# Optimization experiments

Hardware: AMD Instinct MI355X
Metric: run time of the kernel (lower is better)

The kernel has to match this reference:

```python
import jax, jax.numpy as jnp
import numpy as np

B, D, H, W, N = 64, 512, 32, 32, 20
E = 512  # emb_size
TEMP = 10.0


def setup_inputs() -> dict:
    key = jax.random.key(0)
    ks = jax.random.split(key, 16)
    inp = {
        "fvisu": jax.random.normal(ks[0], (B, D, H, W), jnp.float32),
        "fword": jax.random.normal(ks[1], (B, N, D), jnp.float32),
        "context_score": jax.random.uniform(ks[2], (B, N), jnp.float32),
        "fcoord": jax.random.normal(ks[3], (B, 8, H, W), jnp.float32),
        "gest": jax.random.normal(ks[4], (B, 8), jnp.float32),
        "word_mask": jax.random.randint(ks[5], (B, N), 0, 2, jnp.int32),
        # parameters (kaiming-uniform-ish scale)
        "attn_map_w": jax.random.normal(ks[6], (E // 2, D), jnp.float32) * (1.0 / np.sqrt(D)),
        "attn_map_b": jnp.zeros((E // 2,), jnp.float32),
        "attn_score_w": jax.random.normal(ks[7], (1, E // 2), jnp.float32) * (1.0 / np.sqrt(E // 2)),
        "attn_score_b": jnp.zeros((1,), jnp.float32),
        "gamma_w": jax.random.normal(ks[8], (2 * E, D), jnp.float32) * (1.0 / np.sqrt(D)),
        "gamma_b": jnp.zeros((2 * E,), jnp.float32),
        "conv1_w": jax.random.normal(ks[9], (E, D + 8), jnp.float32) * (1.0 / np.sqrt(D + 8)),
        "conv1_b": jnp.zeros((E,), jnp.float32),
    }
    return inp


def mask_softmax(attn_score, word_mask, temp=TEMP):
    # score: (B, N)
    score = jax.nn.softmax(attn_score * temp, axis=1)
    m = word_mask.astype(jnp.int32)
    m = m.at[:, 0].set(0)                      # zero CLS position
    idx = jnp.sum(m, axis=1)                   # index of SEP (post-CLS-zeroing), matches torch loop
    m = m.at[jnp.arange(m.shape[0]), idx].set(0)
    ms = score * m.astype(score.dtype)
    return ms / (jnp.sum(ms, axis=1, keepdims=True) + 1e-8)


def reference(fvisu, fword, context_score, fcoord, gest, word_mask,
              attn_map_w, attn_map_b, attn_score_w, attn_score_b,
              gamma_w, gamma_b, conv1_w, conv1_b):
    # fword: (B, N, D) -> module permutes to (B, D, N)
    fw = jnp.transpose(fword, (0, 2, 1))                      # (B, D, N)
    tile_visu = jnp.mean(fvisu.reshape(B, D, -1), axis=2, keepdims=True)  # (B, D, 1)
    context_tile = tile_visu * fw * context_score[:, None, :]  # (B, D, N)

    # 1x1 Conv1d -> GEMM
    attn_feat = jnp.tanh(jnp.einsum('od,bdn->bon', attn_map_w, context_tile)
                         + attn_map_b[None, :, None])          # (B, E/2, N)
    attn_score = (jnp.einsum('oc,bcn->bon', attn_score_w, attn_feat)[:, 0, :]
                  + attn_score_b[0])                           # (B, N)

    mask_score = mask_softmax(attn_score, word_mask)            # (B, N)
    attn_lang = jnp.einsum('bn,bnd->bd', mask_score, fword)     # (B, D)

    # FiLM parameter decode
    film = attn_lang @ gamma_w.T + gamma_b                      # (B, 2E)
    gammas = jnp.tanh(film[:, :E])[:, :, None, None]
    betas = jnp.tanh(film[:, E:])[:, :, None, None]

    # 1x1 Conv2d on concat(fvisu, fcoord) + InstanceNorm2d (no affine, eps=1e-5)
    x = jnp.concatenate([fvisu, fcoord], axis=1)                # (B, D+8, H, W)
    conv = jnp.einsum('oc,bchw->bohw', conv1_w, x) + conv1_b[None, :, None, None]
    mu = jnp.mean(conv, axis=(2, 3), keepdims=True)
    var = jnp.var(conv, axis=(2, 3), keepdims=True)
    norm = (conv - mu) * jax.lax.rsqrt(var + 1e-5)

    fmodu = jax.nn.relu(gammas * norm + betas)
    fmodu = fvisu + fmodu
    return fmodu, attn_lang, attn_score
```

## Files before the change

### kernel.cpp

```cpp
#include <hip/hip_runtime.h>
#include <math.h>

#define BB 64
#define DD 512
#define HW 1024
#define NN 20
#define EE 512
#define CIN 520
#define KCN 17
#define TEMP_F 10.0f

#define OUT_ALANG (BB*DD*HW)
#define OUT_ASCORE (OUT_ALANG + BB*DD)

typedef __bf16 bf16x8 __attribute__((ext_vector_type(8)));
typedef float f32x4 __attribute__((ext_vector_type(4)));

__device__ __forceinline__ unsigned int pack2bf(float a, float b) {
    unsigned int ua = __builtin_bit_cast(unsigned int, a);
    unsigned int ub = __builtin_bit_cast(unsigned int, b);
    ua += 0x7fffu + ((ua >> 16) & 1u);
    ub += 0x7fffu + ((ub >> 16) & 1u);
    return (ua >> 16) | (ub & 0xffff0000u);
}

__device__ __forceinline__ unsigned short bfr(float x) {
    unsigned int u = __builtin_bit_cast(unsigned int, x);
    u += 0x7fffu + ((u >> 16) & 1u);
    return (unsigned short)(u >> 16);
}

__device__ __forceinline__ float bf2f(unsigned short u) {
    unsigned int x = ((unsigned int)u) << 16;
    return __builtin_bit_cast(float, x);
}

__global__ __launch_bounds__(256) void k_tilevisu(const float* __restrict__ fvisu,
                                                  float* __restrict__ tv) {
    int row = blockIdx.x;
    const float4* p = (const float4*)(fvisu + (size_t)row * HW);
    int tid = threadIdx.x;
    float4 v = p[tid];
    float s = v.x + v.y + v.z + v.w;
    #pragma unroll
    for (int off = 32; off; off >>= 1) s += __shfl_down(s, off, 64);
    __shared__ float part[4];
    if ((tid & 63) == 0) part[tid >> 6] = s;
    __syncthreads();
    if (tid == 0) tv[row] = (part[0] + part[1] + part[2] + part[3]) * (1.0f / HW);
}

__global__ __launch_bounds__(512) void k_convert_x(
    const float* __restrict__ fvisu, const float* __restrict__ fcoord,
    unsigned short* __restrict__ Xf, float* __restrict__ tv) {
    int L = blockIdx.x;
    int kc = L % KCN;
    int b  = L / KCN;
    int t = threadIdx.x;
    int co = t >> 7;
    int tl = t & 127;
    int cbase = kc * 32 + co * 8;
    float sums[8];
    #pragma unroll
    for (int j = 0; j < 8; ++j) sums[j] = 0.f;

    #pragma unroll
    for (int i = 0; i < 2; ++i) {
        int p0 = (tl + 128 * i) * 4;
        float4 f4[8];
        #pragma unroll
        for (int j = 0; j < 8; ++j) {
            int c = cbase + j;
            if (c < DD) {
                f4[j] = *(const float4*)&fvisu[((size_t)b * DD + c) * HW + p0];
            } else if (c < CIN) {
                f4[j] = *(const float4*)&fcoord[((size_t)b * 8 + (c - DD)) * HW + p0];
            } else {
                f4[j] = make_float4(0.f, 0.f, 0.f, 0.f);
            }
        }
        #pragma unroll
        for (int j = 0; j < 8; ++j)
            if (cbase + j < DD) sums[j] += f4[j].x + f4[j].y + f4[j].z + f4[j].w;

        size_t base = (((size_t)b * 64 + (p0 >> 4)) * KCN + kc) * 512
                    + (size_t)(co * 16 + (p0 & 15)) * 8;
        #pragma unroll
        for (int i2 = 0; i2 < 4; ++i2) {
            uint4 v;
            v.x = pack2bf(((const float*)&f4[0])[i2], ((const float*)&f4[1])[i2]);
            v.y = pack2bf(((const float*)&f4[2])[i2], ((const float*)&f4[3])[i2]);
            v.z = pack2bf(((const float*)&f4[4])[i2], ((const float*)&f4[5])[i2]);
            v.w = pack2bf(((const float*)&f4[6])[i2], ((const float*)&f4[7])[i2]);
            *(uint4*)&Xf[base + (size_t)i2 * 8] = v;
        }
    }

    #pragma unroll
    for (int j = 0; j < 8; ++j) {
        float s = sums[j];
        #pragma unroll
        for (int off = 32; off; off >>= 1) s += __shfl_down(s, off, 64);
        sums[j] = s;
    }
    __shared__ float red[8][8];
    int w = t >> 6;
    if ((t & 63) == 0) {
        #pragma unroll
        for (int j = 0; j < 8; ++j) red[w][j] = sums[j];
    }
    __syncthreads();
    if (t < 32) {
        int j = t & 7, c2 = t >> 3;
        int c = kc * 32 + c2 * 8 + j;
        if (c < DD) tv[(size_t)b * DD + c] = (red[c2 * 2][j] + red[c2 * 2 + 1][j]) * (1.0f / HW);
    }
}

__global__ __launch_bounds__(256) void k_convert_w(
    const float* __restrict__ cw, unsigned short* __restrict__ Wf) {
    int t = threadIdx.x;
    int frag = blockIdx.x * 4 + (t >> 6);
    int l = t & 63;
    int M = frag / KCN, kc = frag % KCN;
    int o = M * 16 + (l & 15);
    int k0 = kc * 32 + (l >> 4) * 8;
    float f[8];
    #pragma unroll
    for (int j = 0; j < 8; ++j) {
        int k = k0 + j;
        f[j] = (k < CIN) ? cw[(size_t)o * CIN + k] : 0.f;
    }
    uint4 v;
    v.x = pack2bf(f[0], f[1]);
    v.y = pack2bf(f[2], f[3]);
    v.z = pack2bf(f[4], f[5]);
    v.w = pack2bf(f[6], f[7]);
    *(uint4*)&Wf[(size_t)frag * 512 + (size_t)l * 8] = v;
}

__global__ __launch_bounds__(256) void k_convert_w2(
    const float* __restrict__ amw, unsigned short* __restrict__ Whi,
    unsigned short* __restrict__ Wlo) {
    int t = threadIdx.x;
    int fid = blockIdx.x * 4 + (t >> 6);
    int l = t & 63;
    int ot = fid >> 4, ks = fid & 15;
    int o = ot * 16 + (l & 15);
    int k0 = ks * 32 + ((l >> 4) & 3) * 8;
    float hi[8], lo[8];
    #pragma unroll
    for (int j = 0; j < 8; ++j) {
        float x = amw[(size_t)o * DD + k0 + j];
        unsigned short h = bfr(x);
        hi[j] = bf2f(h);
        lo[j] = x - hi[j];
    }
    uint4 vh, vl;
    vh.x = pack2bf(hi[0], hi[1]); vh.y = pack2bf(hi[2], hi[3]);
    vh.z = pack2bf(hi[4], hi[5]); vh.w = pack2bf(hi[6], hi[7]);
    vl.x = pack2bf(lo[0], lo[1]); vl.y = pack2bf(lo[2], lo[3]);
    vl.z = pack2bf(lo[4], lo[5]); vl.w = pack2bf(lo[6], lo[7]);
    *(uint4*)&Whi[(size_t)fid * 512 + (size_t)l * 8] = vh;
    *(uint4*)&Wlo[(size_t)fid * 512 + (size_t)l * 8] = vl;
}

__global__ __launch_bounds__(256) void k_convert_gwt(
    const float* __restrict__ gw, float* __restrict__ gwT) {
    __shared__ float tile[64][65];
    int bt = blockIdx.x;
    int rt = bt & 15, kt = bt >> 4;
    int t = threadIdx.x;
    int rl = t >> 4;
    int kl = (t & 15) * 4;
    #pragma unroll
    for (int i = 0; i < 4; ++i) {
        int rr = rl + i * 16;
        float4 v = *(const float4*)&gw[(size_t)(rt * 64 + rr) * DD + kt * 64 + kl];
        tile[rr][kl + 0] = v.x; tile[rr][kl + 1] = v.y;
        tile[rr][kl + 2] = v.z; tile[rr][kl + 3] = v.w;
    }
    __syncthreads();
    #pragma unroll
    for (int i = 0; i < 4; ++i) {
        int kk = rl + i * 16;
        float4 v;
        v.x = tile[kl + 0][kk]; v.y = tile[kl + 1][kk];
        v.z = tile[kl + 2][kk]; v.w = tile[kl + 3][kk];
        *(float4*)&gwT[(size_t)(kt * 64 + kk) * 1024 + rt * 64 + kl] = v;
    }
}

__global__ __launch_bounds__(256) void k_attnscore(
    const float* __restrict__ fword, const float* __restrict__ cs,
    const float* __restrict__ tv, const unsigned short* __restrict__ Whi,
    const unsigned short* __restrict__ Wlo, const float* __restrict__ amb,
    const float* __restrict__ asw, const float* __restrict__ asb,
    const int* __restrict__ wmask, float* __restrict__ out_ascore,
    float* __restrict__ out_alang) {
    int b = blockIdx.x;
    __shared__ unsigned short uhi[2][16][64][8];
    __shared__ unsigned short ulo[2][16][64][8];
    __shared__ float scoreP[4][32];
    __shared__ float asc_sh[NN];
    __shared__ float msh[NN];
    int t = threadIdx.x;

    {
        int n = t & 31, kq = t >> 5;
        float csv = (n < NN) ? cs[b * NN + n] : 0.f;
        const float* fwp = fword + ((size_t)b * NN + (n < NN ? n : 0)) * DD;
        const float* tvp = tv + (size_t)b * DD;
        int mt = n >> 4;
        #pragma unroll
        for (int oc = 0; oc < 8; ++oc) {
            int k = kq * 64 + oc * 8;
            float x[8];
            if (n < NN) {
                float4 f0 = *(const float4*)&fwp[k];
                float4 f1 = *(const float4*)&fwp[k + 4];
                float4 t0 = *(const float4*)&tvp[k];
                float4 t1 = *(const float4*)&tvp[k + 4];
                x[0] = f0.x * t0.x * csv; x[1] = f0.y * t0.y * csv;
                x[2] = f0.z * t0.z * csv; x[3] = f0.w * t0.w * csv;
                x[4] = f1.x * t1.x * csv; x[5] = f1.y * t1.y * csv;
                x[6] = f1.z * t1.z * csv; x[7] = f1.w * t1.w * csv;
            } else {
                #pragma unroll
                for (int j = 0; j < 8; ++j) x[j] = 0.f;
            }
            float h[8], lw[8];
            #pragma unroll
            for (int j = 0; j < 8; ++j) {
                h[j] = bf2f(bfr(x[j]));
                lw[j] = x[j] - h[j];
            }
            int ks = k >> 5;
            int l = (n & 15) + ((k >> 3) & 3) * 16;
            uint4 vh, vl;
            vh.x = pack2bf(h[0], h[1]); vh.y = pack2bf(h[2], h[3]);
            vh.z = pack2bf(h[4], h[5]); vh.w = pack2bf(h[6], h[7]);
            vl.x = pack2bf(lw[0], lw[1]); vl.y = pack2bf(lw[2], lw[3]);
            vl.z = pack2bf(lw[4], lw[5]); vl.w = pack2bf(lw[6], lw[7]);
            *(uint4*)&uhi[mt][ks][l][0] = vh;
            *(uint4*)&ulo[mt][ks][l][0] = vl;
        }
    }
    __syncthreads();

    int w = t >> 6, l = t & 63;
    f32x4 acc[2][4];
    #pragma unroll
    for (int mt = 0; mt < 2; ++mt)
        #pragma unroll
        for (int nt = 0; nt < 4; ++nt) acc[mt][nt] = (f32x4){0.f, 0.f, 0.f, 0.f};

    #pragma unroll 4
    for (int ks = 0; ks < 16; ++ks) {
        bf16x8 ah0 = *(const bf16x8*)&uhi[0][ks][l][0];
        bf16x8 ah1 = *(const bf16x8*)&uhi[1][ks][l][0];
        bf16x8 al0 = *(const bf16x8*)&ulo[0][ks][l][0];
        bf16x8 al1 = *(const bf16x8*)&ulo[1][ks][l][0];
        #pragma unroll
        for (int nt = 0; nt < 4; ++nt) {
            size_t fo = ((size_t)((w * 4 + nt) * 16 + ks)) * 512 + (size_t)l * 8;
            bf16x8 bh = *(const bf16x8*)&Whi[fo];
            bf16x8 bl = *(const bf16x8*)&Wlo[fo];
            acc[0][nt] = __builtin_amdgcn_mfma_f32_16x16x32_bf16(ah0, bh, acc[0][nt], 0, 0, 0);
            acc[0][nt] = __builtin_amdgcn_mfma_f32_16x16x32_bf16(al0, bh, acc[0][nt], 0, 0, 0);
            acc[0][nt] = __builtin_amdgcn_mfma_f32_16x16x32_bf16(ah0, bl, acc[0][nt], 0, 0, 0);
            acc[1][nt] = __builtin_amdgcn_mfma_f32_16x16x32_bf16(ah1, bh, acc[1][nt], 0, 0, 0);
            acc[1][nt] = __builtin_amdgcn_mfma_f32_16x16x32_bf16(al1, bh, acc[1][nt], 0, 0, 0);
            acc[1][nt] = __builtin_amdgcn_mfma_f32_16x16x32_bf16(ah1, bl, acc[1][nt], 0, 0, 0);
        }
    }

    float ambv[4], aswv[4];
    #pragma unroll
    for (int nt = 0; nt < 4; ++nt) {
        int o = (w * 4 + nt) * 16 + (l & 15);
        ambv[nt] = amb[o];
        aswv[nt] = asw[o];
    }
    #pragma unroll
    for (int mt = 0; mt < 2; ++mt) {
        #pragma unroll
        for (int j = 0; j < 4; ++j) {
            float p = 0.f;
            #pragma unroll
            for (int nt = 0; nt < 4; ++nt)
                p += aswv[nt] * tanhf(acc[mt][nt][j] + ambv[nt]);
            #pragma unroll
            for (int off = 1; off < 16; off <<= 1) p += __shfl_xor(p, off, 64);
            if ((l & 15) == 0) scoreP[w][mt * 16 + (l >> 4) * 4 + j] = p;
        }
    }
    __syncthreads();
    if (t < NN) {
        float v = scoreP[0][t] + scoreP[1][t] + scoreP[2][t] + scoreP[3][t] + asb[0];
        out_ascore[b * NN + t] = v;
        asc_sh[t] = v;
    }
    __syncthreads();

    if (t == 0) {
        float s[NN];
        float mx = -1e30f;
        for (int n = 0; n < NN; ++n) { s[n] = asc_sh[n] * TEMP_F; mx = fmaxf(mx, s[n]); }
        float se = 0.f;
        for (int n = 0; n < NN; ++n) { s[n] = expf(s[n] - mx); se += s[n]; }
        int m[NN]; int idx = 0;
        for (int n = 0; n < NN; ++n) m[n] = wmask[b * NN + n];
        m[0] = 0;
        for (int n = 0; n < NN; ++n) idx += m[n];
        m[idx] = 0;
        float tot = 0.f;
        for (int n = 0; n < NN; ++n) { float v = (s[n] / se) * (float)m[n]; msh[n] = v; tot += v; }
        float inv = 1.f / (tot + 1e-8f);
        for (int n = 0; n < NN; ++n) msh[n] *= inv;
    }
    __syncthreads();

    #pragma unroll 2
    for (int d = t; d < DD; d += 256) {
        float a = 0.f;
        #pragma unroll
        for (int n = 0; n < NN; ++n) a += msh[n] * fword[((size_t)b * NN + n) * DD + d];
        out_alang[b * DD + d] = a;
    }
}

__global__ __launch_bounds__(256) void k_attnscore_legacy(
    const float* __restrict__ fword, const float* __restrict__ cs,
    const float* __restrict__ tv, const float* __restrict__ amw,
    const float* __restrict__ amb, const float* __restrict__ asw,
    const float* __restrict__ asb, float* __restrict__ out_ascore) {
    int bn = blockIdx.x;
    int b = bn / NN, n = bn % NN;
    __shared__ float u[DD];
    __shared__ float part[4];
    int tid = threadIdx.x;
    float csv = cs[b * NN + n];
    for (int d = tid; d < DD; d += 256)
        u[d] = tv[b * DD + d] * fword[((size_t)b * NN + n) * DD + d] * csv;
    __syncthreads();
    int o = tid;
    const float4* wrow = (const float4*)(amw + (size_t)o * DD);
    const float4* uv = (const float4*)u;
    float dot = 0.f;
    #pragma unroll 4
    for (int i = 0; i < DD / 4; ++i) {
        float4 w4 = wrow[i]; float4 u4 = uv[i];
        dot += w4.x * u4.x + w4.y * u4.y + w4.z * u4.z + w4.w * u4.w;
    }
    float contrib = asw[o] * tanhf(dot + amb[o]);
    #pragma unroll
    for (int off = 32; off; off >>= 1) contrib += __shfl_down(contrib, off, 64);
    if ((tid & 63) == 0) part[tid >> 6] = contrib;
    __syncthreads();
    if (tid == 0) out_ascore[b * NN + n] = part[0] + part[1] + part[2] + part[3] + asb[0];
}

__global__ __launch_bounds__(256) void k_lang_film(
    const float* __restrict__ fword, const int* __restrict__ wmask,
    const float* __restrict__ ascore, const float* __restrict__ gw,
    const float* __restrict__ gb, float* __restrict__ out_alang,
    float* __restrict__ ws_film) {
    int b = blockIdx.x >> 2;
    int qd = blockIdx.x & 3;
    __shared__ float ms[NN];
    __shared__ float al[DD];
    int tid = threadIdx.x;
    if (tid == 0) {
        float s[NN];
        float mx = -1e30f;
        for (int n = 0; n < NN; ++n) { s[n] = ascore[b * NN + n] * TEMP_F; mx = fmaxf(mx, s[n]); }
        float se = 0.f;
        for (int n = 0; n < NN; ++n) { s[n] = expf(s[n] - mx); se += s[n]; }
        int m[NN]; int idx = 0;
        for (int n = 0; n < NN; ++n) m[n] = wmask[b * NN + n];
        m[0] = 0;
        for (int n = 0; n < NN; ++n) idx += m[n];
        m[idx] = 0;
        float tot = 0.f;
        for (int n = 0; n < NN; ++n) { float v = (s[n] / se) * (float)m[n]; ms[n] = v; tot += v; }
        float inv = 1.f / (tot + 1e-8f);
        for (int n = 0; n < NN; ++n) ms[n] *= inv;
    }
    __syncthreads();
    for (int d = tid; d < DD; d += 256) {
        float a = 0.f;
        #pragma unroll
        for (int n = 0; n < NN; ++n) a += ms[n] * fword[((size_t)b * NN + n) * DD + d];
        al[d] = a;
        if (qd == 0) out_alang[b * DD + d] = a;
    }
    __syncthreads();
    {
        int r = qd * 256 + tid;
        const float4* grow = (const float4*)(gw + (size_t)r * DD);
        const float4* av = (const float4*)al;
        float dot = 0.f;
        #pragma unroll 4
        for (int i = 0; i < DD / 4; ++i) {
            float4 g4 = grow[i]; float4 a4 = av[i];
            dot += g4.x * a4.x + g4.y * a4.y + g4.z * a4.z + g4.w * a4.w;
        }
        ws_film[b * 2 * EE + r] = tanhf(dot + gb[r]);
    }
}

__global__ __launch_bounds__(256) void k_film(
    const float* __restrict__ alang, const float* __restrict__ gwT,
    const float* __restrict__ gb, float* __restrict__ ws_film) {
    int b = blockIdx.x;
    __shared__ float al[DD];
    int t = threadIdx.x;
    al[t] = alang[b * DD + t];
    al[t + 256] = alang[b * DD + t + 256];
    __syncthreads();
    float4 acc = make_float4(0.f, 0.f, 0.f, 0.f);
    #pragma unroll 8
    for (int k = 0; k < DD; ++k) {
        float a = al[k];
        float4 g = *(const float4*)&gwT[(size_t)k * 1024 + t * 4];
        acc.x += a * g.x; acc.y += a * g.y; acc.z += a * g.z; acc.w += a * g.w;
    }
    float4 gbv = *(const float4*)&gb[t * 4];
    float4 o;
    o.x = tanhf(acc.x + gbv.x);
    o.y = tanhf(acc.y + gbv.y);
    o.z = tanhf(acc.z + gbv.z);
    o.w = tanhf(acc.w + gbv.w);
    *(float4*)&ws_film[b * 1024 + t * 4] = o;
}

__global__ __launch_bounds__(512, 2) void k_gemm_in_film(
    const unsigned short* __restrict__ Xf, const unsigned short* __restrict__ Wf,
    const float* __restrict__ film, float* __restrict__ out) {
    __shared__ float sP[8][64];
    __shared__ float qP[8][64];
    __shared__ float st[64][4];
    int L = blockIdx.x;
    int ot = (L >> 3) & 7;
    int b  = (L >> 6) * 8 + (L & 7);
    int t = threadIdx.x;
    int w = t >> 6, l = t & 63;

    const unsigned short* Xw = Xf + ((size_t)b * 64 + w * 8) * (KCN * 512) + (size_t)l * 8;
    const unsigned short* Wb = Wf + (size_t)(ot * 4) * (KCN * 512) + (size_t)l * 8;
    int ot2 = 2 * ot;

    f32x4 acc[4][8];
    #pragma unroll
    for (int m = 0; m < 4; ++m)
        #pragma unroll
        for (int n = 0; n < 8; ++n) acc[m][n] = (f32x4){0.f, 0.f, 0.f, 0.f};

    auto kcof = [&](int j) -> int {
        if (j < 15) return j + (j >= ot2 ? 2 : 0);
        return (j == 15) ? ot2 : (ot2 + 1);
    };
    auto loadB = [&](int j, bf16x8* bf_) {
        int kc = kcof(j);
        #pragma unroll
        for (int i = 0; i < 8; ++i)
            bf_[i] = *(const bf16x8*)(Xw + ((size_t)i * KCN + kc) * 512);
    };
    auto loadA = [&](int j, bf16x8* af) {
        int kc = kcof(j);
        #pragma unroll
        for (int m = 0; m < 4; ++m)
            af[m] = *(const bf16x8*)(Wb + ((size_t)m * KCN + kc) * 512);
    };
    auto compute = [&](const bf16x8* af, const bf16x8* bf_) {
        __builtin_amdgcn_s_setprio(1);
        #pragma unroll
        for (int m = 0; m < 4; ++m)
            #pragma unroll
            for (int n = 0; n < 8; ++n)
                acc[m][n] = __builtin_amdgcn_mfma_f32_16x16x32_bf16(af[m], bf_[n], acc[m][n], 0, 0, 0);
        __builtin_amdgcn_s_setprio(0);
    };

    bf16x8 bA[8], bB[8], aA[4], aB[4];
    loadB(0, bA);
    loadA(0, aA);

    #pragma unroll
    for (int j = 0; j < KCN; ++j) {
        if (j & 1) {
            if (j + 1 < KCN) { loadB(j + 1, bA); loadA(j + 1, aA); }
            compute(aB, bB);
        } else {
            if (j + 1 < KCN) { loadB(j + 1, bB); loadA(j + 1, aB); }
            compute(aA, bA);
        }
    }

    #pragma unroll
    for (int m = 0; m < 4; ++m) {
        #pragma unroll
        for (int j = 0; j < 4; ++j) {
            float s = 0.f, q = 0.f;
            #pragma unroll
            for (int n = 0; n < 8; ++n) { float v = acc[m][n][j]; s += v; q += v * v; }
            #pragma unroll
            for (int off = 1; off < 16; off <<= 1) {
                s += __shfl_xor(s, off, 64);
                q += __shfl_xor(q, off, 64);
            }
            if ((l & 15) == 0) {
                int ol = m * 16 + (l >> 4) * 4 + j;
                sP[w][ol] = s;
                qP[w][ol] = q;
            }
        }
    }
    __syncthreads();
    if (t < 64) {
        float s = 0.f, q = 0.f;
        #pragma unroll
        for (int ww = 0; ww < 8; ++ww) { s += sP[ww][t]; q += qP[ww][t]; }
        float mu = s * (1.0f / HW);
        float var = q * (1.0f / HW) - mu * mu;
        int oc = ot * 64 + t;
        st[t][0] = mu;
        st[t][1] = rsqrtf(var + 1e-5f);
        st[t][2] = film[b * 1024 + oc];
        st[t][3] = film[b * 1024 + 512 + oc];
    }
    __syncthreads();

    float* ob = out + ((size_t)b * DD + ot * 64) * HW;
    int q4 = l >> 4;
    #pragma unroll
    for (int m = 0; m < 4; ++m) {
        int kc_m = ot2 + (m >> 1);
        int lp = ((m & 1) * 2 + (q4 >> 1)) * 16 + (l & 15);
        int uo = lp * 8 + (q4 & 1) * 4;
        #pragma unroll
        for (int n = 0; n < 8; ++n) {
            ushort4 rb = *(const ushort4*)(Xf + ((size_t)b * 64 + w * 8 + n) * (KCN * 512)
                                           + ((size_t)kc_m) * 512 + uo);
            int px = w * 128 + n * 16 + (l & 15);
            #pragma unroll
            for (int jj = 0; jj < 4; ++jj) {
                int ol = m * 16 + q4 * 4 + jj;
                f32x4 sv = *(const f32x4*)&st[ol][0];
                float nrm = (acc[m][n][jj] - sv[0]) * sv[1];
                float rr = sv[2] * nrm + sv[3];
                rr = rr > 0.f ? rr : 0.f;
                float res = bf2f(((const unsigned short*)&rb)[jj]);
                ob[(size_t)ol * HW + px] = res + rr;
            }
        }
    }
}

__global__ __launch_bounds__(256) void k_conv_in_film(
    const float* __restrict__ fvisu, const float* __restrict__ fcoord,
    const float* __restrict__ cw, const float* __restrict__ film,
    float* __restrict__ out) {
    int L = blockIdx.x;
    int b = L & 63;
    int tgt = L >> 6;
    int o0 = tgt * 16;
    int tid = threadIdx.x;
    __shared__ float xs[8][HW];
    __shared__ float red[16][4][2];
    __shared__ float stats[16][2];
    float acc[16][4];
    #pragma unroll
    for (int o = 0; o < 16; ++o)
        #pragma unroll
        for (int j = 0; j < 4; ++j) acc[o][j] = 0.f;

    const float* xb_v = fvisu + (size_t)b * DD * HW;
    const float* xb_c = fcoord + (size_t)b * 8 * HW;

    for (int c0 = 0; c0 < CIN; c0 += 8) {
        #pragma unroll
        for (int i = 0; i < 8; ++i) {
            int c = c0 + i;
            const float* src = (c < DD) ? (xb_v + (size_t)c * HW) : (xb_c + (size_t)(c - DD) * HW);
            ((float4*)xs[i])[tid] = ((const float4*)src)[tid];
        }
        __syncthreads();
        #pragma unroll
        for (int i = 0; i < 8; ++i) {
            float xv[4];
            #pragma unroll
            for (int j = 0; j < 4; ++j) xv[j] = xs[i][tid + 256 * j];
            #pragma unroll
            for (int o = 0; o < 16; ++o) {
                float wv = cw[(size_t)(o0 + o) * CIN + (c0 + i)];
                #pragma unroll
                for (int j = 0; j < 4; ++j) acc[o][j] = fmaf(wv, xv[j], acc[o][j]);
            }
        }
        __syncthreads();
    }
    int lane = tid & 63, wid = tid >> 6;
    #pragma unroll
    for (int o = 0; o < 16; ++o) {
        float s = 0.f, q = 0.f;
        #pragma unroll
        for (int j = 0; j < 4; ++j) { s += acc[o][j]; q += acc[o][j] * acc[o][j]; }
        #pragma unroll
        for (int off = 32; off; off >>= 1) {
            s += __shfl_down(s, off, 64);
            q += __shfl_down(q, off, 64);
        }
        if (lane == 0) { red[o][wid][0] = s; red[o][wid][1] = q; }
    }
    __syncthreads();
    if (tid < 16) {
        float s = red[tid][0][0] + red[tid][1][0] + red[tid][2][0] + red[tid][3][0];
        float q = red[tid][0][1] + red[tid][1][1] + red[tid][2][1] + red[tid][3][1];
        float mu = s * (1.0f / HW);
        float var = q * (1.0f / HW) - mu * mu;
        stats[tid][0] = mu;
        stats[tid][1] = rsqrtf(var + 1e-5f);
    }
    __syncthreads();
    #pragma unroll
    for (int o = 0; o < 16; ++o) {
        int oc = o0 + o;
        float mu = stats[o][0], rs = stats[o][1];
        float g  = film[b * 1024 + oc];
        float be = film[b * 1024 + 512 + oc];
        const float* fv = xb_v + (size_t)oc * HW;
        float* op = out + ((size_t)b * DD + oc) * HW;
        #pragma unroll
        for (int j = 0; j < 4; ++j) {
            int p = tid + 256 * j;
            float nrm = (acc[o][j] - mu) * rs;
            float rr = g * nrm + be;
            rr = rr > 0.f ? rr : 0.f;
            op[p] = fv[p] + rr;
        }
    }
}

extern "C" void kernel_launch(void* const* d_in, const int* in_sizes, int n_in,
                              void* d_out, int out_size, void* d_ws, size_t ws_size,
                              hipStream_t stream) {
    const float* fvisu  = (const float*)d_in[0];
    const float* fword  = (const float*)d_in[1];
    const float* cscore = (const float*)d_in[2];
    const float* fcoord = (const float*)d_in[3];
    const int*   wmask  = (const int*)d_in[5];
    const float* amw    = (const float*)d_in[6];
    const float* amb    = (const float*)d_in[7];
    const float* asw    = (const float*)d_in[8];
    const float* asb    = (const float*)d_in[9];
    const float* gw     = (const float*)d_in[10];
    const float* gb     = (const float*)d_in[11];
    const float* cw     = (const float*)d_in[12];

    float* out = (float*)d_out;
    float* ws_tv   = (float*)d_ws;
    float* ws_film = ws_tv + BB * DD;
    unsigned short* Xf  = (unsigned short*)((char*)d_ws + 393216);
    unsigned short* Wf  = (unsigned short*)((char*)d_ws + 393216 + 71303168);
    unsigned short* Whi = (unsigned short*)((char*)d_ws + 393216 + 71303168 + 557056);
    unsigned short* Wlo = Whi + 131072;
    float* gwT = (float*)((char*)d_ws + 393216 + 71303168 + 557056 + 524288);
    const size_t need = 393216 + 71303168 + 557056 + 524288 + 2097152;

    float* out_alang  = out + OUT_ALANG;
    float* out_ascore = out + OUT_ASCORE;

    if (ws_size >= need) {
        k_convert_w<<<136, 256, 0, stream>>>(cw, Wf);
        k_convert_w2<<<64, 256, 0, stream>>>(amw, Whi, Wlo);
        k_convert_gwt<<<128, 256, 0, stream>>>(gw, gwT);
        k_convert_x<<<BB * KCN, 512, 0, stream>>>(fvisu, fcoord, Xf, ws_tv);
        k_attnscore<<<BB, 256, 0, stream>>>(fword, cscore, ws_tv, Whi, Wlo, amb, asw, asb,
                                            wmask, out_ascore, out_alang);
        k_film<<<BB, 256, 0, stream>>>(out_alang, gwT, gb, ws_film);
        k_gemm_in_film<<<512, 512, 0, stream>>>(Xf, Wf, ws_film, out);
    } else {
        k_tilevisu<<<BB * DD, 256, 0, stream>>>(fvisu, ws_tv);
        k_attnscore_legacy<<<BB * NN, 256, 0, stream>>>(fword, cscore, ws_tv, amw, amb, asw, asb, out_ascore);
        k_lang_film<<<BB * 4, 256, 0, stream>>>(fword, wmask, out_ascore, gw, gb, out_alang, ws_film);
        k_conv_in_film<<<BB * 32, 256, 0, stream>>>(fvisu, fcoord, cw, ws_film, out);
    }
}
```

Before: 190.6 us.

## Enlarge GEMM output tile to 128 channels, merge weight-convert kernels, split FiLM

The main conv GEMM now computes 128 output channels per block instead of 64, halving the grid to 256 blocks and doubling the accumulator array to 8x8 MFMA tiles. This halves redundant re-reads of the activation matrix but greatly raises register pressure (the launch-bounds occupancy hint is dropped). It also removes the k-chunk reordering trick. The three parameter-conversion kernels become one launch, and the FiLM kernel is split four ways per batch for more parallelism.

```diff
diff --git a/kernel.cpp b/kernel.cpp
--- a/kernel.cpp
+++ b/kernel.cpp
@@ -117,77 +117,73 @@
     }
 }
 
-__global__ __launch_bounds__(256) void k_convert_w(
-    const float* __restrict__ cw, unsigned short* __restrict__ Wf) {
+__global__ __launch_bounds__(256) void k_convert_params(
+    const float* __restrict__ cw, unsigned short* __restrict__ Wf,
+    const float* __restrict__ amw, unsigned short* __restrict__ Whi,
+    unsigned short* __restrict__ Wlo,
+    const float* __restrict__ gw, float* __restrict__ gwT) {
+    int B0 = blockIdx.x;
     int t = threadIdx.x;
-    int frag = blockIdx.x * 4 + (t >> 6);
-    int l = t & 63;
-    int M = frag / KCN, kc = frag % KCN;
-    int o = M * 16 + (l & 15);
-    int k0 = kc * 32 + (l >> 4) * 8;
-    float f[8];
-    #pragma unroll
-    for (int j = 0; j < 8; ++j) {
-        int k = k0 + j;
-        f[j] = (k < CIN) ? cw[(size_t)o * CIN + k] : 0.f;
-    }
-    uint4 v;
-    v.x = pack2bf(f[0], f[1]);
-    v.y = pack2bf(f[2], f[3]);
-    v.z = pack2bf(f[4], f[5]);
-    v.w = pack2bf(f[6], f[7]);
-    *(uint4*)&Wf[(size_t)frag * 512 + (size_t)l * 8] = v;
-}
-
-__global__ __launch_bounds__(256) void k_convert_w2(
-    const float* __restrict__ amw, unsigned short* __restrict__ Whi,
-    unsigned short* __restrict__ Wlo) {
-    int t = threadIdx.x;
-    int fid = blockIdx.x * 4 + (t >> 6);
-    int l = t & 63;
-    int ot = fid >> 4, ks = fid & 15;
-    int o = ot * 16 + (l & 15);
-    int k0 = ks * 32 + ((l >> 4) & 3) * 8;
-    float hi[8], lo[8];
-    #pragma unroll
-    for (int j = 0; j < 8; ++j) {
-        float x = amw[(size_t)o * DD + k0 + j];
-        unsigned short h = bfr(x);
-        hi[j] = bf2f(h);
-        lo[j] = x - hi[j];
-    }
-    uint4 vh, vl;
-    vh.x = pack2bf(hi[0], hi[1]); vh.y = pack2bf(hi[2], hi[3]);
-    vh.z = pack2bf(hi[4], hi[5]); vh.w = pack2bf(hi[6], hi[7]);
-    vl.x = pack2bf(lo[0], lo[1]); vl.y = pack2bf(lo[2], lo[3]);
-    vl.z = pack2bf(lo[4], lo[5]); vl.w = pack2bf(lo[6], lo[7]);
-    *(uint4*)&Whi[(size_t)fid * 512 + (size_t)l * 8] = vh;
-    *(uint4*)&Wlo[(size_t)fid * 512 + (size_t)l * 8] = vl;
-}
-
-__global__ __launch_bounds__(256) void k_convert_gwt(
-    const float* __restrict__ gw, float* __restrict__ gwT) {
-    __shared__ float tile[64][65];
-    int bt = blockIdx.x;
-    int rt = bt & 15, kt = bt >> 4;
-    int t = threadIdx.x;
-    int rl = t >> 4;
-    int kl = (t & 15) * 4;
-    #pragma unroll
-    for (int i = 0; i < 4; ++i) {
-        int rr = rl + i * 16;
-        float4 v = *(const float4*)&gw[(size_t)(rt * 64 + rr) * DD + kt * 64 + kl];
-        tile[rr][kl + 0] = v.x; tile[rr][kl + 1] = v.y;
-        tile[rr][kl + 2] = v.z; tile[rr][kl + 3] = v.w;
-    }
-    __syncthreads();
-    #pragma unroll
-    for (int i = 0; i < 4; ++i) {
-        int kk = rl + i * 16;
-        float4 v;
-        v.x = tile[kl + 0][kk]; v.y = tile[kl + 1][kk];
-        v.z = tile[kl + 2][kk]; v.w = tile[kl + 3][kk];
-        *(float4*)&gwT[(size_t)(kt * 64 + kk) * 1024 + rt * 64 + kl] = v;
+    if (B0 < 136) {
+        int frag = B0 * 4 + (t >> 6);
+        int l = t & 63;
+        int M = frag / KCN, kc = frag % KCN;
+        int o = M * 16 + (l & 15);
+        int k0 = kc * 32 + (l >> 4) * 8;
+        float f[8];
+        #pragma unroll
+        for (int j = 0; j < 8; ++j) {
+            int k = k0 + j;
+            f[j] = (k < CIN) ? cw[(size_t)o * CIN + k] : 0.f;
+        }
+        uint4 v;
+        v.x = pack2bf(f[0], f[1]);
+        v.y = pack2bf(f[2], f[3]);
+        v.z = pack2bf(f[4], f[5]);
+        v.w = pack2bf(f[6], f[7]);
+        *(uint4*)&Wf[(size_t)frag * 512 + (size_t)l * 8] = v;
+    } else if (B0 < 200) {
+        int fid = (B0 - 136) * 4 + (t >> 6);
+        int l = t & 63;
+        int o = (fid >> 4) * 16 + (l & 15);
+        int k0 = (fid & 15) * 32 + ((l >> 4) & 3) * 8;
+        float hi[8], lo[8];
+        #pragma unroll
+        for (int j = 0; j < 8; ++j) {
+            float x = amw[(size_t)o * DD + k0 + j];
+            unsigned short h = bfr(x);
+            hi[j] = bf2f(h);
+            lo[j] = x - hi[j];
+        }
+        uint4 vh, vl;
+        vh.x = pack2bf(hi[0], hi[1]); vh.y = pack2bf(hi[2], hi[3]);
+        vh.z = pack2bf(hi[4], hi[5]); vh.w = pack2bf(hi[6], hi[7]);
+        vl.x = pack2bf(lo[0], lo[1]); vl.y = pack2bf(lo[2], lo[3]);
+        vl.z = pack2bf(lo[4], lo[5]); vl.w = pack2bf(lo[6], lo[7]);
+        *(uint4*)&Whi[(size_t)fid * 512 + (size_t)l * 8] = vh;
+        *(uint4*)&Wlo[(size_t)fid * 512 + (size_t)l * 8] = vl;
+    } else {
+        __shared__ float tile[64][65];
+        int bt = B0 - 200;
+        int rt = bt & 15, kt = bt >> 4;
+        int rl = t >> 4;
+        int kl = (t & 15) * 4;
+        #pragma unroll
+        for (int i = 0; i < 4; ++i) {
+            int rr = rl + i * 16;
+            float4 v = *(const float4*)&gw[(size_t)(rt * 64 + rr) * DD + kt * 64 + kl];
+            tile[rr][kl + 0] = v.x; tile[rr][kl + 1] = v.y;
+            tile[rr][kl + 2] = v.z; tile[rr][kl + 3] = v.w;
+        }
+        __syncthreads();
+        #pragma unroll
+        for (int i = 0; i < 4; ++i) {
+            int kk = rl + i * 16;
+            float4 v;
+            v.x = tile[kl + 0][kk]; v.y = tile[kl + 1][kk];
+            v.z = tile[kl + 2][kk]; v.w = tile[kl + 3][kk];
+            *(float4*)&gwT[(size_t)(kt * 64 + kk) * 1024 + rt * 64 + kl] = v;
+        }
     }
 }
 
@@ -413,77 +409,63 @@
 __global__ __launch_bounds__(256) void k_film(
     const float* __restrict__ alang, const float* __restrict__ gwT,
     const float* __restrict__ gb, float* __restrict__ ws_film) {
-    int b = blockIdx.x;
+    int b = blockIdx.x >> 2;
+    int q = blockIdx.x & 3;
     __shared__ float al[DD];
     int t = threadIdx.x;
     al[t] = alang[b * DD + t];
     al[t + 256] = alang[b * DD + t + 256];
     __syncthreads();
-    float4 acc = make_float4(0.f, 0.f, 0.f, 0.f);
+    int r = q * 256 + t;
+    float acc = 0.f;
     #pragma unroll 8
-    for (int k = 0; k < DD; ++k) {
-        float a = al[k];
-        float4 g = *(const float4*)&gwT[(size_t)k * 1024 + t * 4];
-        acc.x += a * g.x; acc.y += a * g.y; acc.z += a * g.z; acc.w += a * g.w;
-    }
-    float4 gbv = *(const float4*)&gb[t * 4];
-    float4 o;
-    o.x = tanhf(acc.x + gbv.x);
-    o.y = tanhf(acc.y + gbv.y);
-    o.z = tanhf(acc.z + gbv.z);
-    o.w = tanhf(acc.w + gbv.w);
-    *(float4*)&ws_film[b * 1024 + t * 4] = o;
-}
-
-__global__ __launch_bounds__(512, 2) void k_gemm_in_film(
+    for (int k = 0; k < DD; ++k)
+        acc += al[k] * gwT[(size_t)k * 1024 + r];
+    ws_film[b * 1024 + r] = tanhf(acc + gb[r]);
+}
+
+__global__ __launch_bounds__(512) void k_gemm_in_film(
     const unsigned short* __restrict__ Xf, const unsigned short* __restrict__ Wf,
     const float* __restrict__ film, float* __restrict__ out) {
-    __shared__ float sP[8][64];
-    __shared__ float qP[8][64];
-    __shared__ float st[64][4];
+    __shared__ float sP[8][128];
+    __shared__ float qP[8][128];
+    __shared__ float st[128][4];
     int L = blockIdx.x;
-    int ot = (L >> 3) & 7;
-    int b  = (L >> 6) * 8 + (L & 7);
+    int ot = (L >> 3) & 3;
+    int b  = (L >> 5) * 8 + (L & 7);
     int t = threadIdx.x;
     int w = t >> 6, l = t & 63;
 
     const unsigned short* Xw = Xf + ((size_t)b * 64 + w * 8) * (KCN * 512) + (size_t)l * 8;
-    const unsigned short* Wb = Wf + (size_t)(ot * 4) * (KCN * 512) + (size_t)l * 8;
-    int ot2 = 2 * ot;
-
-    f32x4 acc[4][8];
-    #pragma unroll
-    for (int m = 0; m < 4; ++m)
+    const unsigned short* Wb = Wf + (size_t)(ot * 8) * (KCN * 512) + (size_t)l * 8;
+
+    f32x4 acc[8][8];
+    #pragma unroll
+    for (int m = 0; m < 8; ++m)
         #pragma unroll
         for (int n = 0; n < 8; ++n) acc[m][n] = (f32x4){0.f, 0.f, 0.f, 0.f};
 
-    auto kcof = [&](int j) -> int {
-        if (j < 15) return j + (j >= ot2 ? 2 : 0);
-        return (j == 15) ? ot2 : (ot2 + 1);
-    };
-    auto loadB = [&](int j, bf16x8* bf_) {
-        int kc = kcof(j);
+    auto loadB = [&](int kc, bf16x8* bf_) {
         #pragma unroll
         for (int i = 0; i < 8; ++i)
             bf_[i] = *(const bf16x8*)(Xw + ((size_t)i * KCN + kc) * 512);
     };
-    auto loadA = [&](int j, bf16x8* af) {
-        int kc = kcof(j);
-        #pragma unroll
-        for (int m = 0; m < 4; ++m)
+    auto loadA = [&](int kc, bf16x8* af) {
+        #pragma unroll
+        for (int m = 0; m < 8; ++m)
             af[m] = *(const bf16x8*)(Wb + ((size_t)m * KCN + kc) * 512);
     };
     auto compute = [&](const bf16x8* af, const bf16x8* bf_) {
         __builtin_amdgcn_s_setprio(1);
         #pragma unroll
-        for (int m = 0; m < 4; ++m)
+        for (int m = 0; m < 8; ++m)
             #pragma unroll
             for (int n = 0; n < 8; ++n)
                 acc[m][n] = __builtin_amdgcn_mfma_f32_16x16x32_bf16(af[m], bf_[n], acc[m][n], 0, 0, 0);
         __builtin_amdgcn_s_setprio(0);
     };
 
-    bf16x8 bA[8], bB[8], aA[4], aB[4];
+    bf16x8 bA[8], bB[8], aA[8], aB[8];
     loadB(0, bA);
     loadA(0, aA);
 
@@ -499,7 +481,7 @@
     }
 
     #pragma unroll
-    for (int m = 0; m < 4; ++m) {
+    for (int m = 0; m < 8; ++m) {
         #pragma unroll
         for (int j = 0; j < 4; ++j) {
             float s = 0.f, q = 0.f;
@@ -518,13 +500,13 @@
         }
     }
     __syncthreads();
-    if (t < 64) {
+    if (t < 128) {
         float s = 0.f, q = 0.f;
         #pragma unroll
         for (int ww = 0; ww < 8; ++ww) { s += sP[ww][t]; q += qP[ww][t]; }
         float mu = s * (1.0f / HW);
         float var = q * (1.0f / HW) - mu * mu;
-        int oc = ot * 64 + t;
+        int oc = ot * 128 + t;
         st[t][0] = mu;
         st[t][1] = rsqrtf(var + 1e-5f);
         st[t][2] = film[b * 1024 + oc];
@@ -532,11 +514,11 @@
     }
     __syncthreads();
 
-    float* ob = out + ((size_t)b * DD + ot * 64) * HW;
+    float* ob = out + ((size_t)b * DD + ot * 128) * HW;
     int q4 = l >> 4;
     #pragma unroll
-    for (int m = 0; m < 4; ++m) {
-        int kc_m = ot2 + (m >> 1);
+    for (int m = 0; m < 8; ++m) {
+        int kc_m = 4 * ot + (m >> 1);
         int lp = ((m & 1) * 2 + (q4 >> 1)) * 16 + (l & 15);
         int uo = lp * 8 + (q4 & 1) * 4;
         #pragma unroll
@@ -673,14 +655,12 @@
     float* out_ascore = out + OUT_ASCORE;
 
     if (ws_size >= need) {
-        k_convert_w<<<136, 256, 0, stream>>>(cw, Wf);
-        k_convert_w2<<<64, 256, 0, stream>>>(amw, Whi, Wlo);
-        k_convert_gwt<<<128, 256, 0, stream>>>(gw, gwT);
+        k_convert_params<<<328, 256, 0, stream>>>(cw, Wf, amw, Whi, Wlo, gw, gwT);
         k_convert_x<<<BB * KCN, 512, 0, stream>>>(fvisu, fcoord, Xf, ws_tv);
         k_attnscore<<<BB, 256, 0, stream>>>(fword, cscore, ws_tv, Whi, Wlo, amb, asw, asb,
                                             wmask, out_ascore, out_alang);
-        k_film<<<BB, 256, 0, stream>>>(out_alang, gwT, gb, ws_film);
-        k_gemm_in_film<<<512, 512, 0, stream>>>(Xf, Wf, ws_film, out);
+        k_film<<<BB * 4, 256, 0, stream>>>(out_alang, gwT, gb, ws_film);
+        k_gemm_in_film<<<256, 512, 0, stream>>>(Xf, Wf, ws_film, out);
     } else {
         k_tilevisu<<<BB * DD, 256, 0, stream>>>(fvisu, ws_tv);
         k_attnscore_legacy<<<BB * NN, 256, 0, stream>>>(fword, cscore, ws_tv, amw, amb, asw, asb, out_ascore);
```

New measurement: 736.4 us. +286.4%, slower.
